# Optimization experiments

Measured on AMD Instinct MI355X. Metric: run time of the kernel, lower is better.

## Reference

```python
import jax, jax.numpy as jnp
import numpy as np

B, C, H, W = 32, 512, 24, 8
C8 = C // 8  # PAM query/key channels


def setup_inputs() -> dict:
    key = jax.random.key(0)
    k0, k1, k2, k3, k4 = jax.random.split(key, 5)
    x = jax.random.normal(k0, (B, C, H, W), dtype=jnp.float32)
    Wq = jax.random.normal(k1, (C8, C), dtype=jnp.float32) * 0.02
    bq = jnp.zeros((C8,), dtype=jnp.float32)
    Wk = jax.random.normal(k2, (C8, C), dtype=jnp.float32) * 0.02
    bk = jnp.zeros((C8,), dtype=jnp.float32)
    return {"x": x, "Wq": Wq, "bq": bq, "Wk": Wk, "bk": bk}


def reference(x, Wq, bq, Wk, bk):
    b, c, h, w = x.shape
    hw = h * w
    xf = x.reshape(b, c, hw)  # [B, C, hw]

    # QAConv: einsum('gchw,pcyx->gpyxhw') with kernel == x, then view(B,-1,hw,hw).
    # With m=(h,w) of features and n=(y,x) of kernel this is 'gcm,pcn->gpnm'.
    score = jnp.einsum('gcm,pcn->gpnm', xf, xf)  # [B, B, hw, hw]
    kernel_max = score.max(axis=3)               # max over feature positions -> [B, B, hw]

    # PAM: 1x1 conv projections then bmm(q^T, k).
    q = jnp.einsum('qc,bcm->bqm', Wq, xf) + bq[None, :, None]  # [B, C8, hw]
    k = jnp.einsum('qc,bcm->bqm', Wk, xf) + bk[None, :, None]  # [B, C8, hw]
    energy = jnp.einsum('bqm,bqn->bmn', q, k)                  # [B, hw, hw]
    pos_max = energy.max(axis=2)[None]                         # [1, B, hw]

    return jnp.concatenate([kernel_max, pos_max], axis=0)  # [B+1, B, hw]
```

## Files before the change

### kernel.cpp

```cpp
#include <hip/hip_runtime.h>

typedef __bf16 bf16x8 __attribute__((ext_vector_type(8)));
typedef float f32x4 __attribute__((ext_vector_type(4)));
typedef unsigned short u16x8 __attribute__((ext_vector_type(8)));
typedef unsigned short u16x4 __attribute__((ext_vector_type(4)));

#define B_ 32
#define CC 512
#define HW 192
#define C8_ 64
#define NTRI 528
#define NG3 2112
#define QBUF_B 12288

__device__ inline unsigned short f2bf(float f) {
    unsigned u = __float_as_uint(f);
    unsigned r = (u + 0x7FFFu + ((u >> 16) & 1u)) >> 16;
    return (unsigned short)r;
}

__device__ inline void gload16(const void* g, void* l) {
    __builtin_amdgcn_global_load_lds(
        (const __attribute__((address_space(1))) unsigned*)g,
        (__attribute__((address_space(3))) unsigned*)l,
        16, 0, 0);
}

__global__ void prep(const float* __restrict__ x,
                     const float* __restrict__ Wq, const float* __restrict__ Wk,
                     unsigned short* __restrict__ xt,
                     unsigned short* __restrict__ wqb, unsigned short* __restrict__ wkb) {
    __shared__ unsigned short tile[64 * 64];
    int t = threadIdx.x;
    if (blockIdx.x >= 96) {
        int id = (blockIdx.x - 96) * 8 + blockIdx.y;
        const float* src = (id < 32) ? Wq : Wk;
        unsigned short* dst = (id < 32) ? wqb : wkb;
        int base = (id & 31) * 1024 + t * 4;
        f32x4 a = *(const f32x4*)(src + base);
        u16x4 o;
        #pragma unroll
        for (int e = 0; e < 4; ++e) o[e] = f2bf(a[e]);
        *(u16x4*)(dst + base) = o;
        return;
    }
    int b = blockIdx.x / 3, mt = blockIdx.x % 3;
    int m0 = mt * 64, c0 = blockIdx.y * 64;
    const float* xb = x + (size_t)b * CC * HW + (size_t)c0 * HW + m0;

    int mq = t & 15, cl0 = t >> 4;
    int sw = (mq & 7) << 3;
    #pragma unroll
    for (int rd = 0; rd < 4; ++rd) {
        int cl = rd * 16 + cl0;
        f32x4 v = *(const f32x4*)(xb + cl * HW + mq * 4);
        #pragma unroll
        for (int e = 0; e < 4; ++e)
            tile[(mq * 4 + e) * 64 + (cl ^ sw)] = f2bf(v[e]);
    }
    __syncthreads();
    unsigned short* xo = xt + ((size_t)b * HW + m0) * CC + c0;
    int kc = t & 7, mr0 = t >> 3;
    #pragma unroll
    for (int rd = 0; rd < 2; ++rd) {
        int mr = rd * 32 + mr0;
        u16x8 v = *(const u16x8*)&tile[mr * 64 + ((kc << 3) ^ (((mr >> 2) & 7) << 3))];
        *(u16x8*)(xo + (size_t)mr * CC + kc * 8) = v;
    }
}

__global__ __launch_bounds__(256) void pam_qk(
        const unsigned short* __restrict__ xt,
        const unsigned short* __restrict__ wqb, const unsigned short* __restrict__ wkb,
        const float* __restrict__ bq, const float* __restrict__ bk,
        unsigned short* __restrict__ qo, unsigned short* __restrict__ ko) {
    int b = blockIdx.x, m0 = blockIdx.y * 48;
    int tid = threadIdx.x, w = tid >> 6, lane = tid & 63;
    int l15 = lane & 15, lq = lane >> 4;
    int qc = w * 16 + l15;

    f32x4 accq[3], acck[3];
    #pragma unroll
    for (int i = 0; i < 3; ++i) {
        accq[i] = (f32x4){0.f, 0.f, 0.f, 0.f};
        acck[i] = (f32x4){0.f, 0.f, 0.f, 0.f};
    }

    const unsigned short* xb = xt + ((size_t)b * HW + m0) * CC;
    const unsigned short* wqp = wqb + (size_t)qc * CC;
    const unsigned short* wkp = wkb + (size_t)qc * CC;

    for (int kt = 0; kt < 16; ++kt) {
        int ko8 = kt * 32 + lq * 8;
        bf16x8 wqf = *(const bf16x8*)(wqp + ko8);
        bf16x8 wkf = *(const bf16x8*)(wkp + ko8);
        bf16x8 af[3];
        #pragma unroll
        for (int i = 0; i < 3; ++i)
            af[i] = *(const bf16x8*)(xb + (i * 16 + l15) * CC + ko8);
        #pragma unroll
        for (int i = 0; i < 3; ++i) {
            accq[i] = __builtin_amdgcn_mfma_f32_16x16x32_bf16(af[i], wqf, accq[i], 0, 0, 0);
            acck[i] = __builtin_amdgcn_mfma_f32_16x16x32_bf16(af[i], wkf, acck[i], 0, 0, 0);
        }
    }

    float bqv = bq[qc], bkv = bk[qc];
    #pragma unroll
    for (int i = 0; i < 3; ++i) {
        #pragma unroll
        for (int r = 0; r < 4; ++r) {
            int m = m0 + i * 16 + lq * 4 + r;
            qo[((size_t)b * HW + m) * C8_ + qc] = f2bf(accq[i][r] + bqv);
            ko[((size_t)b * HW + m) * C8_ + qc] = f2bf(acck[i][r] + bkv);
        }
    }
}

__global__ __launch_bounds__(256, 5) void gram3(const unsigned short* __restrict__ xt,
                                                float* __restrict__ ws2) {
    __shared__ __attribute__((aligned(16))) char smem[2 * QBUF_B];

    int tid = threadIdx.x;
    int bid = (blockIdx.x & 7) * 264 + (blockIdx.x >> 3);
    int pairid = bid >> 2, qi = (bid >> 1) & 1, qj = bid & 1;
    int idx = pairid, g = 0;
    while (idx >= B_ - g) { idx -= B_ - g; ++g; }
    int p = g + idx;

    const unsigned short* xga = xt + ((size_t)g * HW + 96 * qi) * CC;
    const unsigned short* xpb = xt + ((size_t)p * HW + 96 * qj) * CC;

    int w = tid >> 6, lane = tid & 63;
    int wr = w >> 1, wc = w & 1;
    int l15 = lane & 15, lq = lane >> 4;

    const unsigned short* sp[3];
    unsigned lo[3];
    #pragma unroll
    for (int ci = 0; ci < 3; ++ci) {
        int q = tid + 256 * ci;
        lo[ci] = (unsigned)q * 16;
        int q2 = (q < 384) ? q : q - 384;
        int r = q2 >> 2, s = q2 & 3;
        sp[ci] = ((q < 384) ? xga : xpb) + r * CC + (((s ^ ((r >> 1) & 3)) << 3));
    }

    unsigned aoff[3], boff[3];
    #pragma unroll
    for (int i = 0; i < 3; ++i) {
        int row = wr * 48 + i * 16 + l15;
        aoff[i] = (unsigned)row * 64 + ((unsigned)(lq ^ ((row >> 1) & 3)) << 4);
    }
    #pragma unroll
    for (int j = 0; j < 3; ++j) {
        int n = wc * 48 + j * 16 + l15;
        boff[j] = 6144u + (unsigned)n * 64 + ((unsigned)(lq ^ ((n >> 1) & 3)) << 4);
    }

    f32x4 acc[3][3];
    #pragma unroll
    for (int i = 0; i < 3; ++i)
        #pragma unroll
        for (int j = 0; j < 3; ++j)
            acc[i][j] = (f32x4){0.f, 0.f, 0.f, 0.f};

    #define STG3(buf, kt)                                                      \
        {                                                                      \
            char* base = smem + (buf) * QBUF_B;                                \
            int k0 = (kt) * 32;                                                \
            gload16(sp[0] + k0, base + lo[0]);                                 \
            gload16(sp[1] + k0, base + lo[1]);                                 \
            gload16(sp[2] + k0, base + lo[2]);                                 \
        }

    #define CMP3(buf)                                                          \
        {                                                                      \
            const char* Bb = smem + (buf) * QBUF_B;                            \
            bf16x8 af[3], bfr[3];                                              \
            _Pragma("unroll")                                                  \
            for (int i = 0; i < 3; ++i)                                        \
                af[i] = *(const bf16x8*)(Bb + aoff[i]);                        \
            _Pragma("unroll")                                                  \
            for (int j = 0; j < 3; ++j)                                        \
                bfr[j] = *(const bf16x8*)(Bb + boff[j]);                       \
            _Pragma("unroll")                                                  \
            for (int i = 0; i < 3; ++i)                                        \
                _Pragma("unroll")                                              \
                for (int j = 0; j < 3; ++j)                                    \
                    acc[i][j] = __builtin_amdgcn_mfma_f32_16x16x32_bf16(       \
                        af[i], bfr[j], acc[i][j], 0, 0, 0);                    \
        }

    STG3(0, 0);
    __syncthreads();
    for (int kt = 0; kt < 16; ++kt) {
        int cur = kt & 1;
        if (kt < 15) STG3(cur ^ 1, kt + 1);
        CMP3(cur);
        __syncthreads();
    }

    float* rowred = (float*)smem;
    float* colred = (float*)(smem + 768);

    #pragma unroll
    for (int i = 0; i < 3; ++i) {
        float rm[4];
        #pragma unroll
        for (int r = 0; r < 4; ++r) rm[r] = -1e30f;
        #pragma unroll
        for (int j = 0; j < 3; ++j)
            #pragma unroll
            for (int r = 0; r < 4; ++r)
                rm[r] = fmaxf(rm[r], acc[i][j][r]);
        #pragma unroll
        for (int msk = 1; msk <= 8; msk <<= 1)
            #pragma unroll
            for (int r = 0; r < 4; ++r)
                rm[r] = fmaxf(rm[r], __shfl_xor(rm[r], msk));
        if (l15 == 0) {
            #pragma unroll
            for (int r = 0; r < 4; ++r)
                rowred[wc * 96 + wr * 48 + i * 16 + lq * 4 + r] = rm[r];
        }
    }
    #pragma unroll
    for (int j = 0; j < 3; ++j) {
        float cm = -1e30f;
        #pragma unroll
        for (int i = 0; i < 3; ++i)
            #pragma unroll
            for (int r = 0; r < 4; ++r)
                cm = fmaxf(cm, acc[i][j][r]);
        cm = fmaxf(cm, __shfl_xor(cm, 16));
        cm = fmaxf(cm, __shfl_xor(cm, 32));
        if (lane < 16) colred[wr * 96 + wc * 48 + j * 16 + l15] = cm;
    }
    __syncthreads();
    float* dst = ws2 + (size_t)(pairid * 4 + qi * 2 + qj) * 192;
    if (tid < 96)
        dst[tid] = fmaxf(rowred[tid], rowred[96 + tid]);
    else if (tid < 192) {
        int n = tid - 96;
        dst[96 + n] = fmaxf(colred[n], colred[96 + n]);
    }
}

__global__ __launch_bounds__(256) void energy_fin(
        const unsigned short* __restrict__ qo,
        const unsigned short* __restrict__ ko,
        const float* __restrict__ ws2,
        float* __restrict__ out) {
    int tid = threadIdx.x;
    if (blockIdx.x >= 128) {
        int pairid = blockIdx.x - 128;
        int idx = pairid, g = 0;
        while (idx >= B_ - g) { idx -= B_ - g; ++g; }
        int p = g + idx;
        const float* wp = ws2 + (size_t)pairid * 768;
        #pragma unroll
        for (int half = 0; half < 2; ++half) {
            int k = half * 256 + tid;
            if (k < 192) {
                int j = k / 96, nn = k % 96;
                out[((size_t)g * B_ + p) * HW + k] =
                    fmaxf(wp[(0 * 2 + j) * 192 + 96 + nn],
                          wp[(1 * 2 + j) * 192 + 96 + nn]);
            } else if (k < 384) {
                int m = k - 192, i = m / 96, mm = m % 96;
                out[((size_t)p * B_ + g) * HW + m] =
                    fmaxf(wp[(i * 2 + 0) * 192 + mm],
                          wp[(i * 2 + 1) * 192 + mm]);
            }
        }
        return;
    }
    int b = blockIdx.x >> 2, m0 = (blockIdx.x & 3) * 48;
    int w = tid >> 6, lane = tid & 63;
    int l15 = lane & 15, lq = lane >> 4;
    int n0 = w * 48;

    f32x4 acc[3][3];
    #pragma unroll
    for (int i = 0; i < 3; ++i)
        #pragma unroll
        for (int j = 0; j < 3; ++j)
            acc[i][j] = (f32x4){0.f, 0.f, 0.f, 0.f};

    const unsigned short* qb = qo + ((size_t)b * HW + m0) * C8_;
    const unsigned short* kb = ko + ((size_t)b * HW + n0) * C8_;

    #pragma unroll
    for (int kt = 0; kt < 2; ++kt) {
        int ko8 = kt * 32 + lq * 8;
        bf16x8 af[3], bfr[3];
        #pragma unroll
        for (int i = 0; i < 3; ++i)
            af[i] = *(const bf16x8*)(qb + (i * 16 + l15) * C8_ + ko8);
        #pragma unroll
        for (int j = 0; j < 3; ++j)
            bfr[j] = *(const bf16x8*)(kb + (j * 16 + l15) * C8_ + ko8);
        #pragma unroll
        for (int i = 0; i < 3; ++i)
            #pragma unroll
            for (int j = 0; j < 3; ++j)
                acc[i][j] = __builtin_amdgcn_mfma_f32_16x16x32_bf16(af[i], bfr[j], acc[i][j], 0, 0, 0);
    }

    __shared__ float red[4][48];
    #pragma unroll
    for (int i = 0; i < 3; ++i) {
        float rm[4];
        #pragma unroll
        for (int r = 0; r < 4; ++r) rm[r] = -1e30f;
        #pragma unroll
        for (int j = 0; j < 3; ++j)
            #pragma unroll
            for (int r = 0; r < 4; ++r)
                rm[r] = fmaxf(rm[r], acc[i][j][r]);
        #pragma unroll
        for (int msk = 1; msk <= 8; msk <<= 1)
            #pragma unroll
            for (int r = 0; r < 4; ++r)
                rm[r] = fmaxf(rm[r], __shfl_xor(rm[r], msk));
        if (l15 == 0) {
            #pragma unroll
            for (int r = 0; r < 4; ++r)
                red[w][i * 16 + lq * 4 + r] = rm[r];
        }
    }
    __syncthreads();
    if (tid < 48) {
        float v = fmaxf(fmaxf(red[0][tid], red[1][tid]),
                        fmaxf(red[2][tid], red[3][tid]));
        out[((size_t)B_ * B_ + b) * HW + m0 + tid] = v;
    }
}

extern "C" void kernel_launch(void* const* d_in, const int* in_sizes, int n_in,
                              void* d_out, int out_size, void* d_ws, size_t ws_size,
                              hipStream_t stream) {
    (void)in_sizes; (void)n_in; (void)out_size; (void)ws_size;
    const float* x  = (const float*)d_in[0];
    const float* Wq = (const float*)d_in[1];
    const float* bq = (const float*)d_in[2];
    const float* Wk = (const float*)d_in[3];
    const float* bk = (const float*)d_in[4];
    float* out = (float*)d_out;

    char* ws = (char*)d_ws;
    unsigned short* xt  = (unsigned short*)ws;
    unsigned short* wqb = (unsigned short*)(ws + 6291456);
    unsigned short* wkb = (unsigned short*)(ws + 6291456 + 65536);
    unsigned short* qbuf = (unsigned short*)(ws + 6291456 + 131072);
    unsigned short* kbuf = (unsigned short*)(ws + 6291456 + 131072 + 786432);
    float* ws2 = (float*)(ws + 6291456 + 131072 + 2 * 786432);

    prep<<<dim3(104, 8), dim3(256), 0, stream>>>(x, Wq, Wk, xt, wqb, wkb);
    pam_qk<<<dim3(32, 4), dim3(256), 0, stream>>>(xt, wqb, wkb, bq, bk, qbuf, kbuf);
    gram3<<<dim3(NG3), dim3(256), 0, stream>>>(xt, ws2);
    energy_fin<<<dim3(656), dim3(256), 0, stream>>>(qbuf, kbuf, ws2, out);
}
```

Before: 60.50 us.

## Tile Gram kernel as 96x192 blocks with 6 waves and triple-buffered LDS pipeline

The cross-batch Gram kernel now assigns each block half of the g rows against all 192 p columns using 384 threads (2x3 waves, 3x4 MFMA tiles per wave), halving the block count and cutting redundant loads of the g-side tile. LDS staging becomes a 3-stage ring with explicit vmcnt waits and a single barrier per k-step instead of a double buffer with two syncs. Row maxima are written straight to the output, and the final kernel only merges two column partials. The trade-off is more registers per wave and lower occupancy (3 blocks per CU) with fewer, larger blocks.

```diff
diff --git a/kernel.cpp b/kernel.cpp
--- a/kernel.cpp
+++ b/kernel.cpp
@@ -10,8 +10,8 @@
 #define HW 192
 #define C8_ 64
 #define NTRI 528
-#define NG3 2112
-#define QBUF_B 12288
+#define NG2 1056
+#define HBUF_B 18432
 
 __device__ inline unsigned short f2bf(float f) {
     unsigned u = __float_as_uint(f);
@@ -117,92 +117,100 @@
     }
 }
 
-__global__ __launch_bounds__(256, 5) void gram3(const unsigned short* __restrict__ xt,
+__global__ __launch_bounds__(384, 3) void gram4(const unsigned short* __restrict__ xt,
+                                                float* __restrict__ out,
                                                 float* __restrict__ ws2) {
-    __shared__ __attribute__((aligned(16))) char smem[2 * QBUF_B];
+    __shared__ __attribute__((aligned(16))) char smem[3 * HBUF_B];
 
     int tid = threadIdx.x;
-    int bid = (blockIdx.x & 7) * 264 + (blockIdx.x >> 3);
-    int pairid = bid >> 2, qi = (bid >> 1) & 1, qj = bid & 1;
+    int bid = (blockIdx.x & 7) * 132 + (blockIdx.x >> 3);
+    int pairid = bid >> 1, h = bid & 1;
     int idx = pairid, g = 0;
     while (idx >= B_ - g) { idx -= B_ - g; ++g; }
     int p = g + idx;
 
-    const unsigned short* xga = xt + ((size_t)g * HW + 96 * qi) * CC;
-    const unsigned short* xpb = xt + ((size_t)p * HW + 96 * qj) * CC;
-
-    int w = tid >> 6, lane = tid & 63;
-    int wr = w >> 1, wc = w & 1;
+    const unsigned short* xga = xt + ((size_t)g * HW + 96 * h) * CC;
+    const unsigned short* xp  = xt + (size_t)p * HW * CC;
+
+    int w = tid / 64, lane = tid & 63;
+    int wr = w / 3, cg = w % 3;
     int l15 = lane & 15, lq = lane >> 4;
 
     const unsigned short* sp[3];
     unsigned lo[3];
     #pragma unroll
     for (int ci = 0; ci < 3; ++ci) {
-        int q = tid + 256 * ci;
+        int q = tid + 384 * ci;
         lo[ci] = (unsigned)q * 16;
         int q2 = (q < 384) ? q : q - 384;
         int r = q2 >> 2, s = q2 & 3;
-        sp[ci] = ((q < 384) ? xga : xpb) + r * CC + (((s ^ ((r >> 1) & 3)) << 3));
-    }
-
-    unsigned aoff[3], boff[3];
+        sp[ci] = ((q < 384) ? xga : xp) + r * CC + ((s ^ ((r >> 1) & 3)) << 3);
+    }
+
+    unsigned aoff[3], boff[4];
     #pragma unroll
     for (int i = 0; i < 3; ++i) {
         int row = wr * 48 + i * 16 + l15;
         aoff[i] = (unsigned)row * 64 + ((unsigned)(lq ^ ((row >> 1) & 3)) << 4);
     }
     #pragma unroll
-    for (int j = 0; j < 3; ++j) {
-        int n = wc * 48 + j * 16 + l15;
+    for (int j = 0; j < 4; ++j) {
+        int n = cg * 64 + j * 16 + l15;
         boff[j] = 6144u + (unsigned)n * 64 + ((unsigned)(lq ^ ((n >> 1) & 3)) << 4);
     }
 
-    f32x4 acc[3][3];
+    f32x4 acc[3][4];
     #pragma unroll
     for (int i = 0; i < 3; ++i)
         #pragma unroll
-        for (int j = 0; j < 3; ++j)
+        for (int j = 0; j < 4; ++j)
             acc[i][j] = (f32x4){0.f, 0.f, 0.f, 0.f};
 
-    #define STG3(buf, kt)                                                      \
+    #define STG4(buf, kt)                                                      \
         {                                                                      \
-            char* base = smem + (buf) * QBUF_B;                                \
+            char* base = smem + (buf) * HBUF_B;                                \
             int k0 = (kt) * 32;                                                \
             gload16(sp[0] + k0, base + lo[0]);                                 \
             gload16(sp[1] + k0, base + lo[1]);                                 \
             gload16(sp[2] + k0, base + lo[2]);                                 \
         }
 
-    #define CMP3(buf)                                                          \
+    #define CMP4(buf)                                                          \
         {                                                                      \
-            const char* Bb = smem + (buf) * QBUF_B;                            \
-            bf16x8 af[3], bfr[3];                                              \
+            const char* Bb = smem + (buf) * HBUF_B;                            \
+            bf16x8 af[3], bfr[4];                                              \
             _Pragma("unroll")                                                  \
             for (int i = 0; i < 3; ++i)                                        \
                 af[i] = *(const bf16x8*)(Bb + aoff[i]);                        \
             _Pragma("unroll")                                                  \
-            for (int j = 0; j < 3; ++j)                                        \
+            for (int j = 0; j < 4; ++j)                                        \
                 bfr[j] = *(const bf16x8*)(Bb + boff[j]);                       \
             _Pragma("unroll")                                                  \
             for (int i = 0; i < 3; ++i)                                        \
                 _Pragma("unroll")                                              \
-                for (int j = 0; j < 3; ++j)                                    \
+                for (int j = 0; j < 4; ++j)                                    \
                     acc[i][j] = __builtin_amdgcn_mfma_f32_16x16x32_bf16(       \
                         af[i], bfr[j], acc[i][j], 0, 0, 0);                    \
         }
 
-    STG3(0, 0);
+    #define WT3() asm volatile("s_waitcnt vmcnt(3)" ::: "memory")
+    #define WT0() asm volatile("s_waitcnt vmcnt(0)" ::: "memory")
+    #define BR()  { __builtin_amdgcn_sched_barrier(0); __builtin_amdgcn_s_barrier(); }
+
+    STG4(0, 0);
+    STG4(1, 1);
+
+    #pragma unroll
+    for (int kt = 0; kt < 16; ++kt) {
+        if (kt < 15) { WT3(); } else { WT0(); }
+        BR();
+        if (kt < 14) STG4((kt + 2) % 3, kt + 2);
+        CMP4(kt % 3);
+    }
     __syncthreads();
-    for (int kt = 0; kt < 16; ++kt) {
-        int cur = kt & 1;
-        if (kt < 15) STG3(cur ^ 1, kt + 1);
-        CMP3(cur);
-        __syncthreads();
-    }
 
     float* rowred = (float*)smem;
-    float* colred = (float*)(smem + 768);
+    float* colred = (float*)(smem + 1152);
 
     #pragma unroll
     for (int i = 0; i < 3; ++i) {
@@ -210,7 +218,7 @@
         #pragma unroll
         for (int r = 0; r < 4; ++r) rm[r] = -1e30f;
         #pragma unroll
-        for (int j = 0; j < 3; ++j)
+        for (int j = 0; j < 4; ++j)
             #pragma unroll
             for (int r = 0; r < 4; ++r)
                 rm[r] = fmaxf(rm[r], acc[i][j][r]);
@@ -222,11 +230,11 @@
         if (l15 == 0) {
             #pragma unroll
             for (int r = 0; r < 4; ++r)
-                rowred[wc * 96 + wr * 48 + i * 16 + lq * 4 + r] = rm[r];
-        }
-    }
-    #pragma unroll
-    for (int j = 0; j < 3; ++j) {
+                rowred[cg * 96 + wr * 48 + i * 16 + lq * 4 + r] = rm[r];
+        }
+    }
+    #pragma unroll
+    for (int j = 0; j < 4; ++j) {
         float cm = -1e30f;
         #pragma unroll
         for (int i = 0; i < 3; ++i)
@@ -235,15 +243,15 @@
                 cm = fmaxf(cm, acc[i][j][r]);
         cm = fmaxf(cm, __shfl_xor(cm, 16));
         cm = fmaxf(cm, __shfl_xor(cm, 32));
-        if (lane < 16) colred[wr * 96 + wc * 48 + j * 16 + l15] = cm;
+        if (lane < 16) colred[wr * 192 + cg * 64 + j * 16 + l15] = cm;
     }
     __syncthreads();
-    float* dst = ws2 + (size_t)(pairid * 4 + qi * 2 + qj) * 192;
-    if (tid < 96)
-        dst[tid] = fmaxf(rowred[tid], rowred[96 + tid]);
-    else if (tid < 192) {
+    if (tid < 96) {
+        float v = fmaxf(fmaxf(rowred[tid], rowred[96 + tid]), rowred[192 + tid]);
+        out[((size_t)p * B_ + g) * HW + 96 * h + tid] = v;
+    } else if (tid < 288) {
         int n = tid - 96;
-        dst[96 + n] = fmaxf(colred[n], colred[96 + n]);
+        ws2[(size_t)pairid * 384 + h * 192 + n] = fmaxf(colred[n], colred[192 + n]);
     }
 }
 
@@ -258,22 +266,9 @@
         int idx = pairid, g = 0;
         while (idx >= B_ - g) { idx -= B_ - g; ++g; }
         int p = g + idx;
-        const float* wp = ws2 + (size_t)pairid * 768;
-        #pragma unroll
-        for (int half = 0; half < 2; ++half) {
-            int k = half * 256 + tid;
-            if (k < 192) {
-                int j = k / 96, nn = k % 96;
-                out[((size_t)g * B_ + p) * HW + k] =
-                    fmaxf(wp[(0 * 2 + j) * 192 + 96 + nn],
-                          wp[(1 * 2 + j) * 192 + 96 + nn]);
-            } else if (k < 384) {
-                int m = k - 192, i = m / 96, mm = m % 96;
-                out[((size_t)p * B_ + g) * HW + m] =
-                    fmaxf(wp[(i * 2 + 0) * 192 + mm],
-                          wp[(i * 2 + 1) * 192 + mm]);
-            }
-        }
+        if (tid < HW)
+            out[((size_t)g * B_ + p) * HW + tid] =
+                fmaxf(ws2[(size_t)pairid * 384 + tid], ws2[(size_t)pairid * 384 + 192 + tid]);
         return;
     }
     int b = blockIdx.x >> 2, m0 = (blockIdx.x & 3) * 48;
@@ -359,6 +354,6 @@
 
     prep<<<dim3(104, 8), dim3(256), 0, stream>>>(x, Wq, Wk, xt, wqb, wkb);
     pam_qk<<<dim3(32, 4), dim3(256), 0, stream>>>(xt, wqb, wkb, bq, bk, qbuf, kbuf);
-    gram3<<<dim3(NG3), dim3(256), 0, stream>>>(xt, ws2);
+    gram4<<<dim3(NG2), dim3(384), 0, stream>>>(xt, out, ws2);
     energy_fin<<<dim3(656), dim3(256), 0, stream>>>(qbuf, kbuf, ws2, out);
 }
```

Result: slower. 65.86 us (+8.9%).
